# Performance work log

Hardware: AMD Instinct MI355X
Metric: run time of the kernel (lower is better)

The kernel has to match this reference:

```python
import jax, jax.numpy as jnp
import numpy as np

B, N, C = 2, 2048, 1024
H = 16
D = C // H  # head_dim = 64
SCALE = D ** -0.5


def setup_inputs() -> dict:
    key = jax.random.key(0)
    ks = jax.random.split(key, 9)
    s = C ** -0.5  # ~ torch Linear default init scale
    return {
        "x": jax.random.normal(ks[0], (B, N, C), dtype=jnp.float32),
        "Wq": jax.random.uniform(ks[1], (C, C), jnp.float32, -s, s),
        "bq": jax.random.uniform(ks[2], (C,), jnp.float32, -s, s),
        "Wk": jax.random.uniform(ks[3], (C, C), jnp.float32, -s, s),
        "bk": jax.random.uniform(ks[4], (C,), jnp.float32, -s, s),
        "Wv": jax.random.uniform(ks[5], (C, C), jnp.float32, -s, s),
        "bv": jax.random.uniform(ks[6], (C,), jnp.float32, -s, s),
        "Wo": jax.random.uniform(ks[7], (C, C), jnp.float32, -s, s),
        "bo": jax.random.uniform(ks[8], (C,), jnp.float32, -s, s),
    }


def reference(x, Wq, bq, Wk, bk, Wv, bv, Wo, bo):
    # Projections: [B,N,C] -> [B,H,N,D]
    def split_heads(t):
        return t.reshape(B, N, H, D).transpose(0, 2, 1, 3)

    q = split_heads(x @ Wq.T + bq)
    k = split_heads(x @ Wk.T + bk)
    v = split_heads(x @ Wv.T + bv)

    scores = jnp.einsum("bhnd,bhmd->bhnm", q, k) * SCALE  # [B,H,N,N]
    attn = jax.nn.softmax(scores, axis=-1)
    out = jnp.einsum("bhnm,bhmd->bhnd", attn, v)  # [B,H,N,D]
    out = out.transpose(0, 2, 1, 3).reshape(B, N, C)
    return out @ Wo.T + bo
```

## Files before the change

kernel.cpp:

```cpp
#include <hip/hip_runtime.h>
#include <stdint.h>


typedef _Float16 h8 __attribute__((ext_vector_type(8)));
typedef _Float16 h4 __attribute__((ext_vector_type(4)));
typedef float f4 __attribute__((ext_vector_type(4)));
typedef float f16f __attribute__((ext_vector_type(16)));
typedef uint32_t u32;
typedef u32 u32x4 __attribute__((ext_vector_type(4)));

#define AS1(p) ((const __attribute__((address_space(1))) void*)(p))
#define AS3(p) ((__attribute__((address_space(3))) void*)(p))

template <int ITERS>
__device__ __forceinline__ void stage128B(const _Float16* g, int ldk, _Float16* s, int tid) {
#pragma unroll
  for (int j = 0; j < ITERS; ++j) {
    int off = j * 4096 + tid * 16;
    int row = off >> 7;
    int ch = (off >> 4) & 7;
    int gch = ch ^ (row & 7);
    __builtin_amdgcn_global_load_lds(AS1(g + row * ldk + gch * 8), AS3(s + (off >> 1)), 16, 0, 0);
  }
}

__device__ __forceinline__ void stage8k(const _Float16* g, int ldk, _Float16* s, int tid) {
  int off = tid * 16;
  int row = off >> 7;
  int ch = (off >> 4) & 7;
  int gch = ch ^ (row & 7);
  __builtin_amdgcn_global_load_lds(AS1(g + row * ldk + gch * 8), AS3(s + (off >> 1)), 16, 0, 0);
}

__device__ __forceinline__ h8 frag64(const _Float16* s, int row, int g) {
  return *(const h8*)(s + row * 64 + ((g ^ (row & 7)) << 3));
}

__global__ void cvt_all(const float* __restrict__ x, const float* __restrict__ Wq,
                        const float* __restrict__ Wk, const float* __restrict__ Wv,
                        const float* __restrict__ Wo, _Float16* __restrict__ xh,
                        _Float16* __restrict__ q, _Float16* __restrict__ k,
                        _Float16* __restrict__ v, _Float16* __restrict__ o) {
  int blk = blockIdx.x;
  const float* src; _Float16* dst; int off;
  if (blk < 4096)      { src = x;  dst = xh; off = blk; }
  else if (blk < 5120) { src = Wq; dst = q;  off = blk - 4096; }
  else if (blk < 6144) { src = Wk; dst = k;  off = blk - 5120; }
  else if (blk < 7168) { src = Wv; dst = v;  off = blk - 6144; }
  else                 { src = Wo; dst = o;  off = blk - 7168; }
  int i = off * 1024 + threadIdx.x * 4;
  f4 vv = *(const f4*)(src + i);
  h4 ov;
  ov[0] = (_Float16)vv[0]; ov[1] = (_Float16)vv[1]; ov[2] = (_Float16)vv[2]; ov[3] = (_Float16)vv[3];
  *(h4*)(dst + i) = ov;
}

__global__ __launch_bounds__(256, 3) void gemm_qkv(
    const _Float16* __restrict__ X,
    const _Float16* __restrict__ W0, const _Float16* __restrict__ W1, const _Float16* __restrict__ W2,
    const float* __restrict__ b0, const float* __restrict__ b1, const float* __restrict__ b2,
    _Float16* __restrict__ O0, _Float16* __restrict__ O1, _Float16* __restrict__ O2) {
  __shared__ _Float16 As[128 * 64];
  __shared__ _Float16 Bs[128 * 64];
  int z = blockIdx.z;
  const _Float16* W = (z == 0) ? W0 : (z == 1) ? W1 : W2;
  const float* bias = (z == 0) ? b0 : (z == 1) ? b1 : b2;

  int tid = threadIdx.x;
  int lane = tid & 63, wave = tid >> 6;
  int quad = lane >> 4, l15 = lane & 15;
  int wm = (wave >> 1) << 6, wn = (wave & 1) << 6;
  int m0 = blockIdx.y << 7, n0 = blockIdx.x << 7;

  f4 acc[4][4] = {};
  for (int k0 = 0; k0 < 1024; k0 += 64) {
    stage128B<4>(X + m0 * 1024 + k0, 1024, As, tid);
    stage128B<4>(W + n0 * 1024 + k0, 1024, Bs, tid);
    __syncthreads();
#pragma unroll
    for (int ks = 0; ks < 2; ++ks) {
      h8 af[4], bf[4];
#pragma unroll
      for (int i = 0; i < 4; ++i) af[i] = frag64(As, wm + i * 16 + l15, ks * 4 + quad);
#pragma unroll
      for (int i = 0; i < 4; ++i) bf[i] = frag64(Bs, wn + i * 16 + l15, ks * 4 + quad);
#pragma unroll
      for (int mi = 0; mi < 4; ++mi)
#pragma unroll
        for (int ni = 0; ni < 4; ++ni)
          acc[mi][ni] = __builtin_amdgcn_mfma_f32_16x16x32_f16(af[mi], bf[ni], acc[mi][ni], 0, 0, 0);
    }
    __syncthreads();
  }

  if (z == 2) {
#pragma unroll
    for (int mi = 0; mi < 4; ++mi) {
#pragma unroll
      for (int ni = 0; ni < 4; ++ni) {
        int o = n0 + wn + ni * 16 + l15;
        float bv = bias[o];
        int h = o >> 6, dd = o & 63;
        int m = m0 + wm + mi * 16 + quad * 4;
        int b = m >> 11, n = m & 2047;
        h4 v;
#pragma unroll
        for (int r = 0; r < 4; ++r) v[r] = (_Float16)(acc[mi][ni][r] + bv);
        *(h4*)(O2 + (((b * 16 + h) * 64 + dd) * 2048 + n)) = v;
      }
    }
  } else {
    float scale = (z == 0) ? 0.125f * 1.44269504089f : 1.0f;
    _Float16* Out = (z == 0) ? O0 : O1;
#pragma unroll
    for (int mi = 0; mi < 4; ++mi) {
#pragma unroll
      for (int ni = 0; ni < 4; ++ni) {
        int o = n0 + wn + ni * 16 + l15;
        float bv = bias[o];
        int h = o >> 6, d = o & 63;
#pragma unroll
        for (int r = 0; r < 4; ++r) {
          int m = m0 + wm + mi * 16 + quad * 4 + r;
          int b = m >> 11, n = m & 2047;
          float v = (acc[mi][ni][r] + bv) * scale;
          Out[(((b * 16 + h) * 2048 + n) << 6) + d] = (_Float16)v;
        }
      }
    }
  }
}

__global__ __launch_bounds__(256, 3) void gemm_out(
    const _Float16* __restrict__ A, const _Float16* __restrict__ W,
    const float* __restrict__ bias, float* __restrict__ Out) {
  __shared__ _Float16 As[128 * 64];
  __shared__ _Float16 Bs[64 * 64];
  int tid = threadIdx.x;
  int lane = tid & 63, wave = tid >> 6;
  int quad = lane >> 4, l15 = lane & 15;
  int wm = (wave >> 1) << 6, wn = (wave & 1) << 5;
  int m0 = blockIdx.y << 7, n0 = blockIdx.x << 6;

  f4 acc[4][2] = {};
  for (int k0 = 0; k0 < 1024; k0 += 64) {
    stage128B<4>(A + m0 * 1024 + k0, 1024, As, tid);
    stage128B<2>(W + n0 * 1024 + k0, 1024, Bs, tid);
    __syncthreads();
#pragma unroll
    for (int ks = 0; ks < 2; ++ks) {
      h8 af[4], bf[2];
#pragma unroll
      for (int i = 0; i < 4; ++i) af[i] = frag64(As, wm + i * 16 + l15, ks * 4 + quad);
#pragma unroll
      for (int i = 0; i < 2; ++i) bf[i] = frag64(Bs, wn + i * 16 + l15, ks * 4 + quad);
#pragma unroll
      for (int mi = 0; mi < 4; ++mi)
#pragma unroll
        for (int ni = 0; ni < 2; ++ni)
          acc[mi][ni] = __builtin_amdgcn_mfma_f32_16x16x32_f16(af[mi], bf[ni], acc[mi][ni], 0, 0, 0);
    }
    __syncthreads();
  }
#pragma unroll
  for (int mi = 0; mi < 4; ++mi) {
#pragma unroll
    for (int ni = 0; ni < 2; ++ni) {
      int o = n0 + wn + ni * 16 + l15;
      float bv = bias[o];
#pragma unroll
      for (int r = 0; r < 4; ++r) {
        int m = m0 + wm + mi * 16 + quad * 4 + r;
        Out[m * 1024 + o] = acc[mi][ni][r] + bv;
      }
    }
  }
}

__global__ __launch_bounds__(512, 4) void attn(
    const _Float16* __restrict__ Q, const _Float16* __restrict__ Kv,
    const _Float16* __restrict__ Vt, _Float16* __restrict__ AO) {
  __shared__ _Float16 smem[6 * 4096];
  _Float16* Ksb = smem;
  _Float16* Vsb = smem + 3 * 4096;

  int tid = threadIdx.x, lane = tid & 63, wave = tid >> 6;
  int h = lane >> 5, l31 = lane & 31;
  int p = wave & 1, qg = wave >> 1;
  int bh = blockIdx.y, q0 = blockIdx.x << 7;

  const _Float16* Qb = Q + (bh * 2048 + q0 + qg * 32 + l31) * 64;
  h8 qf[4];
#pragma unroll
  for (int ks4 = 0; ks4 < 4; ++ks4)
    qf[ks4] = *(const h8*)(Qb + ks4 * 16 + h * 8);

  int krow = (l31 & 19) | ((l31 & 4) << 1) | ((l31 & 8) >> 1);
  int kbase = (p * 32 + krow) * 64;
  int kx = krow & 7;
  int vx = l31 & 7;

  const _Float16* Kb = Kv + bh * 131072;
  const _Float16* Vb = Vt + bh * 131072;
  f16f oacc[2] = {};
  float lsum = 0.f;

  stage8k(Kb, 64, Ksb, tid);
  stage8k(Vb, 2048, Vsb, tid);
  stage8k(Kb + 4096, 64, Ksb + 4096, tid);
  stage8k(Vb + 64, 2048, Vsb + 4096, tid);

  int bp = 0;
  for (int ph = 0; ph < 32; ++ph) {
    __syncthreads();
    if (ph < 30) {
      int sl = bp ? bp - 1 : 2;
      int pr = ph + 2;
      stage8k(Kb + pr * 4096, 64, Ksb + sl * 4096, tid);
      stage8k(Vb + pr * 64, 2048, Vsb + sl * 4096, tid);
    }
    const _Float16* Kst = Ksb + bp * 4096;
    const _Float16* Vst = Vsb + bp * 4096;

    f16f sacc = {};
#pragma unroll
    for (int ks4 = 0; ks4 < 4; ++ks4) {
      h8 kf = *(const h8*)(Kst + kbase + (((ks4 * 2 + h) ^ kx) << 3));
      sacc = __builtin_amdgcn_mfma_f32_32x32x16_f16(kf, qf[ks4], sacc, 0, 0, 0);
    }

    u32 pkw[8];
#pragma unroll
    for (int i = 0; i < 8; ++i) {
      float pa = __builtin_amdgcn_exp2f(sacc[2 * i]);
      float pb = __builtin_amdgcn_exp2f(sacc[2 * i + 1]);
      lsum += pa + pb;
      pkw[i] = __builtin_bit_cast(u32, __builtin_amdgcn_cvt_pkrtz(pa, pb));
    }

#pragma unroll
    for (int s = 0; s < 2; ++s) {
      u32x4 pw = {pkw[4 * s], pkw[4 * s + 1], pkw[4 * s + 2], pkw[4 * s + 3]};
      h8 pb = __builtin_bit_cast(h8, pw);
      int ch = (((p << 2) | (s << 1) | h) ^ vx) << 3;
#pragma unroll
      for (int dt = 0; dt < 2; ++dt) {
        h8 vf = *(const h8*)(Vst + (dt * 32 + l31) * 64 + ch);
        oacc[dt] = __builtin_amdgcn_mfma_f32_32x32x16_f16(vf, pb, oacc[dt], 0, 0, 0);
      }
    }
    bp = (bp == 2) ? 0 : bp + 1;
  }

  __syncthreads();
  float* cb = (float*)smem;
  if (p) {
    float* w = cb + (qg * 64 + lane) * 33;
#pragma unroll
    for (int i = 0; i < 16; ++i) w[i] = oacc[0][i];
#pragma unroll
    for (int i = 0; i < 16; ++i) w[16 + i] = oacc[1][i];
    w[32] = lsum;
  }
  __syncthreads();
  if (!p) {
    const float* r = cb + (qg * 64 + lane) * 33;
#pragma unroll
    for (int i = 0; i < 16; ++i) oacc[0][i] += r[i];
#pragma unroll
    for (int i = 0; i < 16; ++i) oacc[1][i] += r[16 + i];
    lsum += r[32];

    float l = lsum + __shfl_xor(lsum, 32);
    float inv = 1.0f / l;
    int b = bh >> 4, hh = bh & 15;
    int n = q0 + qg * 32 + l31;
    _Float16* base = AO + (b * 2048 + n) * 1024 + hh * 64;
#pragma unroll
    for (int dt = 0; dt < 2; ++dt) {
#pragma unroll
      for (int b2 = 0; b2 < 4; ++b2) {
        h4 o;
#pragma unroll
        for (int a = 0; a < 4; ++a) o[a] = (_Float16)(oacc[dt][b2 * 4 + a] * inv);
        *(h4*)(base + dt * 32 + b2 * 8 + h * 4) = o;
      }
    }
  }
}

extern "C" void kernel_launch(void* const* d_in, const int* in_sizes, int n_in,
                              void* d_out, int out_size, void* d_ws, size_t ws_size,
                              hipStream_t stream) {
  const float* x = (const float*)d_in[0];
  const float* Wq = (const float*)d_in[1];
  const float* bq = (const float*)d_in[2];
  const float* Wk = (const float*)d_in[3];
  const float* bk = (const float*)d_in[4];
  const float* Wv = (const float*)d_in[5];
  const float* bv = (const float*)d_in[6];
  const float* Wo = (const float*)d_in[7];
  const float* bo = (const float*)d_in[8];
  float* out = (float*)d_out;

  char* w = (char*)d_ws;
  _Float16* xh  = (_Float16*)(w);
  _Float16* Wqh = (_Float16*)(w + (8u << 20));
  _Float16* Wkh = (_Float16*)(w + (10u << 20));
  _Float16* Wvh = (_Float16*)(w + (12u << 20));
  _Float16* Woh = (_Float16*)(w + (14u << 20));
  _Float16* Qh  = (_Float16*)(w + (16u << 20));
  _Float16* Kh  = (_Float16*)(w + (24u << 20));
  _Float16* Vth = (_Float16*)(w + (32u << 20));
  _Float16* AOh = xh;

  cvt_all<<<8192, 256, 0, stream>>>(x, Wq, Wk, Wv, Wo, xh, Wqh, Wkh, Wvh, Woh);
  gemm_qkv<<<dim3(8, 32, 3), 256, 0, stream>>>(xh, Wqh, Wkh, Wvh, bq, bk, bv, Qh, Kh, Vth);
  attn<<<dim3(16, 32), 512, 0, stream>>>(Qh, Kh, Vth, AOh);
  gemm_out<<<dim3(16, 32), 256, 0, stream>>>(AOh, Woh, bo, out);
}
```

Before: 183.9 us.

## Switch attention K/V staging to double buffering and raise occupancy target

Attention K/V tiles now use two LDS buffers instead of three, prefetching one tile ahead rather than two, which cuts shared memory per block. Launch bounds move to 8 blocks per CU so more waves can hide latency. The K swizzle is changed to a different XOR pattern to avoid bank conflicts for the permuted row mapping. The shorter prefetch distance may expose more global-load latency per iteration, and the higher occupancy target limits registers per thread.

```diff
diff --git a/kernel.cpp b/kernel.cpp
--- a/kernel.cpp
+++ b/kernel.cpp
@@ -24,12 +24,19 @@
   }
 }
 
-__device__ __forceinline__ void stage8k(const _Float16* g, int ldk, _Float16* s, int tid) {
+__device__ __forceinline__ void stage8k_v(const _Float16* g, _Float16* s, int tid) {
   int off = tid * 16;
   int row = off >> 7;
   int ch = (off >> 4) & 7;
   int gch = ch ^ (row & 7);
-  __builtin_amdgcn_global_load_lds(AS1(g + row * ldk + gch * 8), AS3(s + (off >> 1)), 16, 0, 0);
+  __builtin_amdgcn_global_load_lds(AS1(g + row * 2048 + gch * 8), AS3(s + (off >> 1)), 16, 0, 0);
+}
+__device__ __forceinline__ void stage8k_k(const _Float16* g, _Float16* s, int tid) {
+  int off = tid * 16;
+  int row = off >> 7;
+  int ch = (off >> 4) & 7;
+  int gch = ch ^ ((row & 3) | ((row >> 1) & 4));
+  __builtin_amdgcn_global_load_lds(AS1(g + row * 64 + gch * 8), AS3(s + (off >> 1)), 16, 0, 0);
 }
 
 __device__ __forceinline__ h8 frag64(const _Float16* s, int row, int g) {
@@ -177,12 +184,12 @@
   }
 }
 
-__global__ __launch_bounds__(512, 4) void attn(
+__global__ __launch_bounds__(512, 8) void attn(
     const _Float16* __restrict__ Q, const _Float16* __restrict__ Kv,
     const _Float16* __restrict__ Vt, _Float16* __restrict__ AO) {
-  __shared__ _Float16 smem[6 * 4096];
+  __shared__ _Float16 smem[4 * 4096 + 512];
   _Float16* Ksb = smem;
-  _Float16* Vsb = smem + 3 * 4096;
+  _Float16* Vsb = smem + 2 * 4096;
 
   int tid = threadIdx.x, lane = tid & 63, wave = tid >> 6;
   int h = lane >> 5, l31 = lane & 31;
@@ -197,7 +204,7 @@
 
   int krow = (l31 & 19) | ((l31 & 4) << 1) | ((l31 & 8) >> 1);
   int kbase = (p * 32 + krow) * 64;
-  int kx = krow & 7;
+  int kx = (krow & 3) | ((krow >> 1) & 4);
   int vx = l31 & 7;
 
   const _Float16* Kb = Kv + bh * 131072;
@@ -205,22 +212,18 @@
   f16f oacc[2] = {};
   float lsum = 0.f;
 
-  stage8k(Kb, 64, Ksb, tid);
-  stage8k(Vb, 2048, Vsb, tid);
-  stage8k(Kb + 4096, 64, Ksb + 4096, tid);
-  stage8k(Vb + 64, 2048, Vsb + 4096, tid);
-
-  int bp = 0;
+  stage8k_k(Kb, Ksb, tid);
+  stage8k_v(Vb, Vsb, tid);
+
   for (int ph = 0; ph < 32; ++ph) {
-    __syncthreads();
-    if (ph < 30) {
-      int sl = bp ? bp - 1 : 2;
-      int pr = ph + 2;
-      stage8k(Kb + pr * 4096, 64, Ksb + sl * 4096, tid);
-      stage8k(Vb + pr * 64, 2048, Vsb + sl * 4096, tid);
-    }
-    const _Float16* Kst = Ksb + bp * 4096;
-    const _Float16* Vst = Vsb + bp * 4096;
+    int cur = ph & 1;
+    __syncthreads();
+    if (ph < 31) {
+      stage8k_k(Kb + (ph + 1) * 4096, Ksb + ((cur ^ 1) << 12), tid);
+      stage8k_v(Vb + (ph + 1) * 64, Vsb + ((cur ^ 1) << 12), tid);
+    }
+    const _Float16* Kst = Ksb + (cur << 12);
+    const _Float16* Vst = Vsb + (cur << 12);
 
     f16f sacc = {};
 #pragma unroll
@@ -249,7 +252,6 @@
         oacc[dt] = __builtin_amdgcn_mfma_f32_32x32x16_f16(vf, pb, oacc[dt], 0, 0, 0);
       }
     }
-    bp = (bp == 2) ? 0 : bp + 1;
   }
 
   __syncthreads();
```

After: 284.6 us. 1.55x slower.
